# Kernel optimization log

Measured on AMD Instinct MI355X. Metric: run time of the kernel, lower is better.

## Reference

```python
import jax, jax.numpy as jnp
import numpy as np

DIM = 384
NUM_HEADS = 6
HEAD_DIM = DIM // NUM_HEADS
MLP_HIDDEN = 4 * DIM
SCALE = HEAD_DIM ** -0.5
EPS = 1e-5


def layer_norm(x, w, b):
    mu = jnp.mean(x, axis=-1, keepdims=True)
    var = jnp.mean(jnp.square(x - mu), axis=-1, keepdims=True)
    return (x - mu) * jax.lax.rsqrt(var + EPS) * w + b


def setup_inputs() -> dict:
    key = jax.random.key(0)
    ks = jax.random.split(key, 24)
    d = DIM
    s = 0.02
    inp = {
        'x1': jax.random.normal(ks[0], (16, d, 32, 32), jnp.float32),
        'x2': jax.random.normal(ks[1], (16, d, 32, 32), jnp.float32),
        # per-branch attention-input LayerNorm + kqv projection (no bias)
        'ln_a1_w': jnp.ones((d,), jnp.float32), 'ln_a1_b': jnp.zeros((d,), jnp.float32),
        'kqv1_w': jax.random.normal(ks[2], (d, 3 * d), jnp.float32) * s,
        'ln_a2_w': jnp.ones((d,), jnp.float32), 'ln_a2_b': jnp.zeros((d,), jnp.float32),
        'kqv2_w': jax.random.normal(ks[3], (d, 3 * d), jnp.float32) * s,
        # output projections
        'proj1_w': jax.random.normal(ks[4], (d, d), jnp.float32) * s,
        'proj1_b': jnp.zeros((d,), jnp.float32),
        'proj2_w': jax.random.normal(ks[5], (d, d), jnp.float32) * s,
        'proj2_b': jnp.zeros((d,), jnp.float32),
        # post-attention LayerNorms
        'ln1_w': jnp.ones((d,), jnp.float32), 'ln1_b': jnp.zeros((d,), jnp.float32),
        'ln2_w': jnp.ones((d,), jnp.float32), 'ln2_b': jnp.zeros((d,), jnp.float32),
        # MLPs
        'mlp1_fc1_w': jax.random.normal(ks[6], (d, MLP_HIDDEN), jnp.float32) * s,
        'mlp1_fc1_b': jnp.zeros((MLP_HIDDEN,), jnp.float32),
        'mlp1_fc2_w': jax.random.normal(ks[7], (MLP_HIDDEN, d), jnp.float32) * s,
        'mlp1_fc2_b': jnp.zeros((d,), jnp.float32),
        'mlp2_fc1_w': jax.random.normal(ks[8], (d, MLP_HIDDEN), jnp.float32) * s,
        'mlp2_fc1_b': jnp.zeros((MLP_HIDDEN,), jnp.float32),
        'mlp2_fc2_w': jax.random.normal(ks[9], (MLP_HIDDEN, d), jnp.float32) * s,
        'mlp2_fc2_b': jnp.zeros((d,), jnp.float32),
    }
    return inp


def _kqv_branch(x, ln_w, ln_b, Wkqv):
    # x: [B, C, H, W] -> embedding [B, N, C]; k,q,v: [B, h, N, hd]
    B, C, H, W = x.shape
    N = H * W
    emb = x.reshape(B, C, N).transpose(0, 2, 1)
    xn = layer_norm(emb, ln_w, ln_b)
    kqv = (xn @ Wkqv).reshape(B, N, 3, NUM_HEADS, HEAD_DIM).transpose(2, 0, 3, 1, 4)
    return kqv[0], kqv[1], kqv[2], emb


def _cross_attn(q, k, v):
    # q,k,v: [B, h, N, hd] -> [B, N, C]
    scores = jnp.einsum('bhnd,bhmd->bhnm', q, k) * SCALE
    a = jax.nn.softmax(scores, axis=-1)
    o = jnp.einsum('bhnm,bhmd->bhnd', a, v)
    B, h, N, hd = o.shape
    return o.transpose(0, 2, 1, 3).reshape(B, N, h * hd)


def reference(x1, x2, ln_a1_w, ln_a1_b, kqv1_w, ln_a2_w, ln_a2_b, kqv2_w,
              proj1_w, proj1_b, proj2_w, proj2_b, ln1_w, ln1_b, ln2_w, ln2_b,
              mlp1_fc1_w, mlp1_fc1_b, mlp1_fc2_w, mlp1_fc2_b,
              mlp2_fc1_w, mlp2_fc1_b, mlp2_fc2_w, mlp2_fc2_b):
    B, C, H, W = x1.shape
    k1, q1, v1, emb1 = _kqv_branch(x1, ln_a1_w, ln_a1_b, kqv1_w)
    k2, q2, v2, emb2 = _kqv_branch(x2, ln_a2_w, ln_a2_b, kqv2_w)
    a1 = _cross_attn(q1, k2, v2)   # branch 1 queries attend to branch 2
    a2 = _cross_attn(q2, k1, v1)
    out1 = emb1 + (a1 @ proj1_w + proj1_b)
    h1 = layer_norm(out1, ln1_w, ln1_b)
    out1 = out1 + (jax.nn.gelu(h1 @ mlp1_fc1_w + mlp1_fc1_b, approximate=False) @ mlp1_fc2_w + mlp1_fc2_b)
    out2 = emb2 + (a2 @ proj2_w + proj2_b)
    h2 = layer_norm(out2, ln2_w, ln2_b)
    out2 = out2 + (jax.nn.gelu(h2 @ mlp2_fc1_w + mlp2_fc1_b, approximate=False) @ mlp2_fc2_w + mlp2_fc2_b)
    out1 = out1.transpose(0, 2, 1).reshape(B, C, H, W)
    out2 = out2.transpose(0, 2, 1).reshape(B, C, H, W)
    return (out1, out2)
```

## Files before the change

### kernel.cpp

```cpp
#include <hip/hip_runtime.h>
#include <math.h>

typedef unsigned short u16;
typedef __attribute__((ext_vector_type(8))) short short8;
typedef __attribute__((ext_vector_type(4))) float f32x4;

#define MFMA(a,b,c) __builtin_amdgcn_mfma_f32_16x16x32_bf16(a, b, c, 0, 0, 0)
#define SWZ(row, ch) ((((ch) ^ ((row) & 7)) << 3))

__device__ __forceinline__ float b2f(u16 v) {
    union { unsigned int i; float f; } c; c.i = ((unsigned int)v) << 16; return c.f;
}
__device__ __forceinline__ u16 f2b(float f) {
    union { float f; unsigned int i; } c; c.f = f;
    unsigned int u = c.i;
    return (u16)((u + 0x7fffu + ((u >> 16) & 1u)) >> 16);
}

struct TWArgs { const float* src[8]; u16* dst[8]; int K[8]; int N[8]; };

__global__ __launch_bounds__(256) void transpose_w(TWArgs a) {
    int wi = blockIdx.z;
    int K = a.K[wi], N = a.N[wi];
    int n0 = blockIdx.x * 32, k0 = blockIdx.y * 32;
    if (n0 >= N || k0 >= K) return;
    __shared__ float t[32][33];
    const float* s = a.src[wi]; u16* d = a.dst[wi];
    int tx = threadIdx.x & 31, ty = threadIdx.x >> 5;
    for (int i = 0; i < 32; i += 8)
        t[ty + i][tx] = s[(size_t)(k0 + ty + i) * N + n0 + tx];
    __syncthreads();
    for (int i = 0; i < 32; i += 8)
        d[(size_t)(n0 + ty + i) * K + k0 + tx] = f2b(t[tx][ty + i]);
}

__global__ __launch_bounds__(256)
void ln_tr(const float* __restrict__ x0, const float* __restrict__ x1,
           const float* __restrict__ w0, const float* __restrict__ bb0,
           const float* __restrict__ w1, const float* __restrict__ bb1,
           u16* __restrict__ xn0, u16* __restrict__ xn1) {
    int br = blockIdx.z;
    const float* x  = br ? x1 : x0;
    const float* wv = br ? w1 : w0;
    const float* bv = br ? bb1 : bb0;
    u16* xn = br ? xn1 : xn0;
    int b = blockIdx.y, n0 = blockIdx.x * 32;
    __shared__ float tile[32][385];
    __shared__ float smu[32], srs[32];
    int tid = threadIdx.x;
    const float* xb = x + (size_t)b * 384 * 1024 + n0;
    for (int idx = tid; idx < 384 * 32; idx += 256) {
        int c = idx >> 5, nn = idx & 31;
        tile[nn][c] = xb[(size_t)c * 1024 + nn];
    }
    __syncthreads();
    {
        int nn = tid >> 3, part = tid & 7;
        float s1 = 0.f, s2 = 0.f;
        for (int c = part * 48; c < part * 48 + 48; ++c) {
            float v = tile[nn][c]; s1 += v; s2 += v * v;
        }
        for (int off = 1; off < 8; off <<= 1) {
            s1 += __shfl_xor(s1, off, 64); s2 += __shfl_xor(s2, off, 64);
        }
        if (part == 0) {
            float mu = s1 * (1.f / 384.f);
            float var = s2 * (1.f / 384.f) - mu * mu;
            smu[nn] = mu; srs[nn] = rsqrtf(fmaxf(var, 0.f) + 1e-5f);
        }
    }
    __syncthreads();
    size_t rowbase = (size_t)b * 1024 + n0;
    for (int idx = tid; idx < 32 * 384; idx += 256) {
        int nn = idx / 384, c = idx - nn * 384;
        float v = tile[nn][c];
        float g = (v - smu[nn]) * srs[nn] * wv[c] + bv[c];
        xn[(rowbase + nn) * 384 + c] = f2b(g);
    }
}

__global__ __launch_bounds__(256)
void ln_rows(const float* __restrict__ i0, const float* __restrict__ i1,
             const float* __restrict__ w0, const float* __restrict__ bb0,
             const float* __restrict__ w1, const float* __restrict__ bb1,
             u16* __restrict__ o0, u16* __restrict__ o1) {
    int br = blockIdx.z;
    const float* in = br ? i1 : i0;
    const float* wv = br ? w1 : w0;
    const float* bv = br ? bb1 : bb0;
    u16* out = br ? o1 : o0;
    int w = threadIdx.x >> 6, l = threadIdx.x & 63;
    size_t row = (size_t)blockIdx.x * 4 + w;
    const float* p = in + row * 384;
    float v[6]; float s1 = 0.f, s2 = 0.f;
    #pragma unroll
    for (int j = 0; j < 6; j++) { v[j] = p[j * 64 + l]; s1 += v[j]; s2 += v[j] * v[j]; }
    for (int off = 1; off < 64; off <<= 1) {
        s1 += __shfl_xor(s1, off, 64); s2 += __shfl_xor(s2, off, 64);
    }
    float mu = s1 * (1.f / 384.f);
    float var = s2 * (1.f / 384.f) - mu * mu;
    float rs = rsqrtf(fmaxf(var, 0.f) + 1e-5f);
    #pragma unroll
    for (int j = 0; j < 6; j++) {
        int c = j * 64 + l;
        out[row * 384 + c] = f2b((v[j] - mu) * rs * wv[c] + bv[c]);
    }
}

template <int EPI>
__global__ __launch_bounds__(256)
void gemm128(const u16* __restrict__ A0, const u16* __restrict__ A1,
             const u16* __restrict__ B0, const u16* __restrict__ B1,
             void* C0v, void* C1v,
             const float* __restrict__ bias0, const float* __restrict__ bias1,
             const void* R0v, const void* R1v,
             int N, int K) {
    const int br = blockIdx.z;
    const u16* A = br ? A1 : A0;
    const u16* B = br ? B1 : B0;
    void* Cv = br ? C1v : C0v;
    const float* bias = br ? bias1 : bias0;
    const void* Rv = br ? R1v : R0v;

    const int n0 = blockIdx.x * 128;
    const int m0 = blockIdx.y * 128;
    const int tid = threadIdx.x;
    const int w = tid >> 6, l = tid & 63;
    const int wm = w >> 1, wn = w & 1;
    const int lr = l & 15, lq = l >> 4;

    __shared__ alignas(16) u16 As[2][128 * 40];
    __shared__ alignas(16) u16 Bs[2][128 * 40];

    f32x4 acc[4][4];
    #pragma unroll
    for (int i = 0; i < 4; i++)
        #pragma unroll
        for (int j = 0; j < 4; j++) acc[i][j] = (f32x4)0.0f;

    const int ar0 = tid >> 2, ac0 = (tid & 3) * 8;
    const int ar1 = ar0 + 64;
    const u16* Ap0 = A + (size_t)(m0 + ar0) * K + ac0;
    const u16* Ap1 = A + (size_t)(m0 + ar1) * K + ac0;
    const u16* Bp0 = B + (size_t)(n0 + ar0) * K + ac0;
    const u16* Bp1 = B + (size_t)(n0 + ar1) * K + ac0;

    const int nk = K >> 5;
    uint4 pa0 = *(const uint4*)Ap0, pa1 = *(const uint4*)Ap1;
    uint4 pb0 = *(const uint4*)Bp0, pb1 = *(const uint4*)Bp1;
    *(uint4*)&As[0][ar0 * 40 + ac0] = pa0;
    *(uint4*)&As[0][ar1 * 40 + ac0] = pa1;
    *(uint4*)&Bs[0][ar0 * 40 + ac0] = pb0;
    *(uint4*)&Bs[0][ar1 * 40 + ac0] = pb1;
    pa0 = *(const uint4*)(Ap0 + 32); pa1 = *(const uint4*)(Ap1 + 32);
    pb0 = *(const uint4*)(Bp0 + 32); pb1 = *(const uint4*)(Bp1 + 32);
    __syncthreads();

    for (int kt = 0; kt < nk; ++kt) {
        const int cur = kt & 1;
        if (kt + 1 < nk) {
            const int nx = cur ^ 1;
            *(uint4*)&As[nx][ar0 * 40 + ac0] = pa0;
            *(uint4*)&As[nx][ar1 * 40 + ac0] = pa1;
            *(uint4*)&Bs[nx][ar0 * 40 + ac0] = pb0;
            *(uint4*)&Bs[nx][ar1 * 40 + ac0] = pb1;
        }
        if (kt + 2 < nk) {
            const int kb = (kt + 2) * 32;
            pa0 = *(const uint4*)(Ap0 + kb); pa1 = *(const uint4*)(Ap1 + kb);
            pb0 = *(const uint4*)(Bp0 + kb); pb1 = *(const uint4*)(Bp1 + kb);
        }
        short8 af[4], bf[4];
        #pragma unroll
        for (int mt = 0; mt < 4; ++mt)
            af[mt] = *(const short8*)&As[cur][(wm * 64 + mt * 16 + lr) * 40 + lq * 8];
        #pragma unroll
        for (int nt = 0; nt < 4; ++nt)
            bf[nt] = *(const short8*)&Bs[cur][(wn * 64 + nt * 16 + lr) * 40 + lq * 8];
        #pragma unroll
        for (int mt = 0; mt < 4; ++mt)
            #pragma unroll
            for (int nt = 0; nt < 4; ++nt)
                acc[mt][nt] = MFMA(af[mt], bf[nt], acc[mt][nt]);
        __syncthreads();
    }

    #pragma unroll
    for (int mt = 0; mt < 4; ++mt)
        #pragma unroll
        for (int nt = 0; nt < 4; ++nt) {
            const int col = n0 + wn * 64 + nt * 16 + lr;
            const int rbase = m0 + wm * 64 + mt * 16 + lq * 4;
            const float bv = (EPI == 0) ? 0.f : bias[col];
            #pragma unroll
            for (int r = 0; r < 4; r++) {
                const int row = rbase + r;
                const size_t idx = (size_t)row * N + col;
                float v = acc[mt][nt][r];
                if (EPI == 0) {
                    if (col < 768) {
                        ((u16*)Cv)[idx] = f2b(col >= 384 ? v * 0.125f : v);
                    } else {
                        u16* vtb = (u16*)Rv;
                        vtb[((((size_t)(row >> 10)) * 6 + ((col - 768) >> 6)) * 64
                             + (col & 63)) * 1024 + (row & 1023)] = f2b(v);
                    }
                } else if (EPI == 1) {
                    float xr = ((const float*)Rv)[
                        ((size_t)(row >> 10) * 384 + col) * 1024 + (row & 1023)];
                    ((float*)Cv)[idx] = v + bv + xr;
                } else if (EPI == 2) {
                    v += bv;
                    float g = 0.5f * v * (1.f + erff(v * 0.70710678118f));
                    ((u16*)Cv)[idx] = f2b(g);
                } else {
                    ((float*)Cv)[idx] = v + bv + ((const float*)Rv)[idx];
                }
            }
        }
}

__global__ __launch_bounds__(256)
void attn_k(const u16* __restrict__ kqvA, const u16* __restrict__ kqvB,
            const u16* __restrict__ vtA, const u16* __restrict__ vtB,
            u16* __restrict__ oA, u16* __restrict__ oB) {
    const int z = blockIdx.z, b = z >> 1, ob = z & 1;
    const int h = blockIdx.y, qb = blockIdx.x;
    const u16* kqvQ  = (ob ? kqvB : kqvA) + (size_t)b * 1024 * 1152;
    const u16* kqvKV = (ob ? kqvA : kqvB) + (size_t)b * 1024 * 1152;
    const u16* vt    = (ob ? vtA : vtB) + ((size_t)b * 6 + h) * 64 * 1024;
    u16* outp = (ob ? oB : oA) + (size_t)b * 1024 * 384;
    const u16* qp = kqvQ + 384 + h * 64;
    const u16* kp = kqvKV + h * 64;

    __shared__ alignas(16) u16 Qs[128 * 64];
    __shared__ alignas(16) u16 Ks[64 * 64];
    __shared__ alignas(16) u16 Vts[64 * 64];
    __shared__ alignas(16) u16 Ps[4 * 32 * 64];

    const int tid = threadIdx.x, w = tid >> 6, l = tid & 63;
    const int lr = l & 15, lq = l >> 4;
    u16* Psw = Ps + w * 32 * 64;

    #pragma unroll
    for (int i = 0; i < 4; i++) {
        int s = tid + i * 256, row = s >> 3, ch = s & 7;
        *(uint4*)&Qs[row * 64 + SWZ(row, ch)] =
            *(const uint4*)&qp[(size_t)(qb * 128 + row) * 1152 + ch * 8];
    }

    const int srow = tid >> 3, sch = tid & 7;
    uint4 kpre[2], vpre[2];
    #pragma unroll
    for (int i = 0; i < 2; i++) {
        int row = srow + i * 32;
        kpre[i] = *(const uint4*)&kp[(size_t)row * 1152 + sch * 8];
        vpre[i] = *(const uint4*)&vt[(size_t)row * 1024 + sch * 8];
    }

    f32x4 oacc[2][4];
    float psum[2][4];
    #pragma unroll
    for (int a = 0; a < 2; a++)
        #pragma unroll
        for (int n = 0; n < 4; n++) oacc[a][n] = (f32x4)0.0f;
    #pragma unroll
    for (int a = 0; a < 2; a++)
        #pragma unroll
        for (int r = 0; r < 4; r++) psum[a][r] = 0.f;

    for (int jt = 0; jt < 16; ++jt) {
        #pragma unroll
        for (int i = 0; i < 2; i++) {
            int row = srow + i * 32;
            int o = row * 64 + SWZ(row, sch);
            *(uint4*)&Ks[o] = kpre[i];
            *(uint4*)&Vts[o] = vpre[i];
        }
        __syncthreads();
        if (jt < 15) {
            #pragma unroll
            for (int i = 0; i < 2; i++) {
                int row = srow + i * 32;
                kpre[i] = *(const uint4*)&kp[(size_t)((jt + 1) * 64 + row) * 1152 + sch * 8];
                vpre[i] = *(const uint4*)&vt[(size_t)row * 1024 + (jt + 1) * 64 + sch * 8];
            }
        }

        f32x4 sacc[2][4];
        #pragma unroll
        for (int a = 0; a < 2; a++)
            #pragma unroll
            for (int n = 0; n < 4; n++) sacc[a][n] = (f32x4)0.0f;
        #pragma unroll
        for (int ks = 0; ks < 2; ++ks) {
            short8 aq[2], bk[4];
            #pragma unroll
            for (int a = 0; a < 2; a++) {
                int row = w * 32 + a * 16 + lr;
                aq[a] = *(const short8*)&Qs[row * 64 + SWZ(row, ks * 4 + lq)];
            }
            #pragma unroll
            for (int n = 0; n < 4; n++) {
                int row = n * 16 + lr;
                bk[n] = *(const short8*)&Ks[row * 64 + SWZ(row, ks * 4 + lq)];
            }
            #pragma unroll
            for (int a = 0; a < 2; a++)
                #pragma unroll
                for (int n = 0; n < 4; n++) sacc[a][n] = MFMA(aq[a], bk[n], sacc[a][n]);
        }

        #pragma unroll
        for (int a = 0; a < 2; a++)
            #pragma unroll
            for (int r = 0; r < 4; r++) {
                int prow = a * 16 + lq * 4 + r;
                float ps = 0.f;
                #pragma unroll
                for (int n = 0; n < 4; n++) {
                    float p = __expf(sacc[a][n][r]);
                    ps += p;
                    Psw[prow * 64 + ((((2 * n + (lr >> 3)) ^ (prow & 7)) << 3) + (lr & 7))] = f2b(p);
                }
                psum[a][r] += ps;
            }

        #pragma unroll
        for (int ks = 0; ks < 2; ++ks) {
            short8 ap[2], bv4[4];
            #pragma unroll
            for (int a = 0; a < 2; a++) {
                int row = a * 16 + lr;
                ap[a] = *(const short8*)&Psw[row * 64 + SWZ(row, ks * 4 + lq)];
            }
            #pragma unroll
            for (int n = 0; n < 4; n++) {
                int row = n * 16 + lr;
                bv4[n] = *(const short8*)&Vts[row * 64 + SWZ(row, ks * 4 + lq)];
            }
            #pragma unroll
            for (int a = 0; a < 2; a++)
                #pragma unroll
                for (int n = 0; n < 4; n++) oacc[a][n] = MFMA(ap[a], bv4[n], oacc[a][n]);
        }
        __syncthreads();
    }

    #pragma unroll
    for (int a = 0; a < 2; a++)
        #pragma unroll
        for (int r = 0; r < 4; r++) {
            float s = psum[a][r];
            s += __shfl_xor(s, 1, 64); s += __shfl_xor(s, 2, 64);
            s += __shfl_xor(s, 4, 64); s += __shfl_xor(s, 8, 64);
            psum[a][r] = s;
        }
    #pragma unroll
    for (int a = 0; a < 2; a++)
        #pragma unroll
        for (int n = 0; n < 4; n++)
            #pragma unroll
            for (int r = 0; r < 4; r++) {
                size_t row = (size_t)qb * 128 + w * 32 + a * 16 + lq * 4 + r;
                int col = h * 64 + n * 16 + lr;
                outp[row * 384 + col] = f2b(oacc[a][n][r] / psum[a][r]);
            }
}

__global__ __launch_bounds__(256)
void transpose_out(const float* __restrict__ r0, const float* __restrict__ r1,
                   float* __restrict__ out) {
    int z = blockIdx.z, ob = z >> 4, b = z & 15;
    const float* rp = ob ? r1 : r0;
    int c0 = blockIdx.y * 32, n0 = blockIdx.x * 32;
    __shared__ float t[32][33];
    int tx = threadIdx.x & 31, ty = threadIdx.x >> 5;
    for (int i = 0; i < 32; i += 8)
        t[ty + i][tx] = rp[((size_t)b * 1024 + n0 + ty + i) * 384 + c0 + tx];
    __syncthreads();
    for (int i = 0; i < 32; i += 8)
        out[(size_t)ob * 6291456 + ((size_t)b * 384 + c0 + ty + i) * 1024 + n0 + tx]
            = t[tx][ty + i];
}

extern "C" void kernel_launch(void* const* d_in, const int* in_sizes, int n_in,
                              void* d_out, int out_size, void* d_ws, size_t ws_size,
                              hipStream_t stream) {
    const float* x1      = (const float*)d_in[0];
    const float* x2      = (const float*)d_in[1];
    const float* ln_a1_w = (const float*)d_in[2];
    const float* ln_a1_b = (const float*)d_in[3];
    const float* kqv1_w  = (const float*)d_in[4];
    const float* ln_a2_w = (const float*)d_in[5];
    const float* ln_a2_b = (const float*)d_in[6];
    const float* kqv2_w  = (const float*)d_in[7];
    const float* proj1_w = (const float*)d_in[8];
    const float* proj1_b = (const float*)d_in[9];
    const float* proj2_w = (const float*)d_in[10];
    const float* proj2_b = (const float*)d_in[11];
    const float* ln1_w   = (const float*)d_in[12];
    const float* ln1_b   = (const float*)d_in[13];
    const float* ln2_w   = (const float*)d_in[14];
    const float* ln2_b   = (const float*)d_in[15];
    const float* m1f1w   = (const float*)d_in[16];
    const float* m1f1b   = (const float*)d_in[17];
    const float* m1f2w   = (const float*)d_in[18];
    const float* m1f2b   = (const float*)d_in[19];
    const float* m2f1w   = (const float*)d_in[20];
    const float* m2f1b   = (const float*)d_in[21];
    const float* m2f2w   = (const float*)d_in[22];
    const float* m2f2b   = (const float*)d_in[23];
    (void)in_sizes; (void)n_in; (void)out_size; (void)ws_size;

    const size_t R = 16384;
    char* ws = (char*)d_ws;
    size_t off = 0;
    auto alloc = [&](size_t bytes) -> char* {
        char* p = ws + off;
        off = (off + bytes + 255) & ~(size_t)255;
        return p;
    };
    u16* kqv1t  = (u16*)alloc(1152 * 384 * 2);
    u16* kqv2t  = (u16*)alloc(1152 * 384 * 2);
    u16* proj1t = (u16*)alloc(384 * 384 * 2);
    u16* proj2t = (u16*)alloc(384 * 384 * 2);
    u16* fc11t  = (u16*)alloc(1536 * 384 * 2);
    u16* fc12t  = (u16*)alloc(1536 * 384 * 2);
    u16* fc21t  = (u16*)alloc(384 * 1536 * 2);
    u16* fc22t  = (u16*)alloc(384 * 1536 * 2);
    u16* xn1 = (u16*)alloc(R * 384 * 2);
    u16* xn2 = (u16*)alloc(R * 384 * 2);
    char* regC = alloc(R * 1152 * 2 * 2);
    u16* kqv1 = (u16*)regC;
    u16* kqv2 = (u16*)(regC + R * 1152 * 2);
    float* oa1 = (float*)regC;
    float* oa2 = (float*)(regC + R * 384 * 4);
    u16* hid_b2 = (u16*)(regC + 2 * R * 384 * 4);
    u16* at1 = (u16*)d_out;
    u16* at2 = at1 + R * 384;
    u16* vt1 = at2 + R * 384;
    u16* vt2 = vt1 + (size_t)16 * 6 * 64 * 1024;
    u16* hid_b1 = (u16*)d_out;

    TWArgs tw;
    tw.src[0] = kqv1_w;  tw.dst[0] = kqv1t;  tw.K[0] = 384;  tw.N[0] = 1152;
    tw.src[1] = kqv2_w;  tw.dst[1] = kqv2t;  tw.K[1] = 384;  tw.N[1] = 1152;
    tw.src[2] = proj1_w; tw.dst[2] = proj1t; tw.K[2] = 384;  tw.N[2] = 384;
    tw.src[3] = proj2_w; tw.dst[3] = proj2t; tw.K[3] = 384;  tw.N[3] = 384;
    tw.src[4] = m1f1w;   tw.dst[4] = fc11t;  tw.K[4] = 384;  tw.N[4] = 1536;
    tw.src[5] = m2f1w;   tw.dst[5] = fc12t;  tw.K[5] = 384;  tw.N[5] = 1536;
    tw.src[6] = m1f2w;   tw.dst[6] = fc21t;  tw.K[6] = 1536; tw.N[6] = 384;
    tw.src[7] = m2f2w;   tw.dst[7] = fc22t;  tw.K[7] = 1536; tw.N[7] = 384;
    transpose_w<<<dim3(48, 48, 8), dim3(256), 0, stream>>>(tw);

    ln_tr<<<dim3(32, 16, 2), dim3(256), 0, stream>>>(
        x1, x2, ln_a1_w, ln_a1_b, ln_a2_w, ln_a2_b, xn1, xn2);

    gemm128<0><<<dim3(9, 128, 2), dim3(256), 0, stream>>>(
        xn1, xn2, kqv1t, kqv2t, (void*)kqv1, (void*)kqv2,
        (const float*)nullptr, (const float*)nullptr,
        (const void*)vt1, (const void*)vt2, 1152, 384);

    attn_k<<<dim3(8, 6, 32), dim3(256), 0, stream>>>(kqv1, kqv2, vt1, vt2, at1, at2);

    gemm128<1><<<dim3(3, 128, 2), dim3(256), 0, stream>>>(
        at1, at2, proj1t, proj2t, (void*)oa1, (void*)oa2,
        proj1_b, proj2_b, (const void*)x1, (const void*)x2, 384, 384);

    ln_rows<<<dim3(4096, 1, 2), dim3(256), 0, stream>>>(
        oa1, oa2, ln1_w, ln1_b, ln2_w, ln2_b, xn1, xn2);

    for (int half = 0; half < 2; ++half) {
        const size_t ro = (size_t)half * 8192;
        gemm128<2><<<dim3(12, 64, 2), dim3(256), 0, stream>>>(
            xn1 + ro * 384, xn2 + ro * 384, fc11t, fc12t,
            (void*)hid_b1, (void*)hid_b2, m1f1b, m2f1b, nullptr, nullptr, 1536, 384);
        gemm128<3><<<dim3(3, 64, 2), dim3(256), 0, stream>>>(
            hid_b1, hid_b2, fc21t, fc22t,
            (void*)(oa1 + ro * 384), (void*)(oa2 + ro * 384),
            m1f2b, m2f2b, (const void*)(oa1 + ro * 384), (const void*)(oa2 + ro * 384),
            384, 1536);
    }

    transpose_out<<<dim3(32, 12, 32), dim3(256), 0, stream>>>(oa1, oa2, (float*)d_out);
}
```

Before: 649.7 us.

## Deepen K/V prefetch, remap attention grid for XCD locality, use exp2 softmax

```diff
diff --git a/kernel.cpp b/kernel.cpp
--- a/kernel.cpp
+++ b/kernel.cpp
@@ -7,6 +7,7 @@
 
 #define MFMA(a,b,c) __builtin_amdgcn_mfma_f32_16x16x32_bf16(a, b, c, 0, 0, 0)
 #define SWZ(row, ch) ((((ch) ^ ((row) & 7)) << 3))
+#define EXP2F(x) __builtin_amdgcn_exp2f(x)
 
 __device__ __forceinline__ float b2f(u16 v) {
     union { unsigned int i; float f; } c; c.i = ((unsigned int)v) << 16; return c.f;
@@ -15,6 +16,10 @@
     union { float f; unsigned int i; } c; c.f = f;
     unsigned int u = c.i;
     return (u16)((u + 0x7fffu + ((u >> 16) & 1u)) >> 16);
+}
+__device__ __forceinline__ u16 f2b_p(float f) {
+    union { float f; unsigned int i; } c; c.f = f;
+    return (u16)((c.i + 0x8000u) >> 16);
 }
 
 struct TWArgs { const float* src[8]; u16* dst[8]; int K[8]; int N[8]; };
@@ -200,7 +205,7 @@
                 float v = acc[mt][nt][r];
                 if (EPI == 0) {
                     if (col < 768) {
-                        ((u16*)Cv)[idx] = f2b(col >= 384 ? v * 0.125f : v);
+                        ((u16*)Cv)[idx] = f2b(col >= 384 ? v * 0.18033688f : v);
                     } else {
                         u16* vtb = (u16*)Rv;
                         vtb[((((size_t)(row >> 10)) * 6 + ((col - 768) >> 6)) * 64
@@ -225,8 +230,11 @@
 void attn_k(const u16* __restrict__ kqvA, const u16* __restrict__ kqvB,
             const u16* __restrict__ vtA, const u16* __restrict__ vtB,
             u16* __restrict__ oA, u16* __restrict__ oB) {
-    const int z = blockIdx.z, b = z >> 1, ob = z & 1;
-    const int h = blockIdx.y, qb = blockIdx.x;
+    const int bid = blockIdx.x;
+    const int g = bid & 7, qb = (bid >> 3) & 7, s = bid >> 6;
+    const int grp = s * 8 + g;
+    const int ob = grp & 1, h = (grp >> 1) % 6, b = grp / 12;
+
     const u16* kqvQ  = (ob ? kqvB : kqvA) + (size_t)b * 1024 * 1152;
     const u16* kqvKV = (ob ? kqvA : kqvB) + (size_t)b * 1024 * 1152;
     const u16* vt    = (ob ? vtA : vtB) + ((size_t)b * 6 + h) * 64 * 1024;
@@ -245,19 +253,21 @@
 
     #pragma unroll
     for (int i = 0; i < 4; i++) {
-        int s = tid + i * 256, row = s >> 3, ch = s & 7;
+        int si = tid + i * 256, row = si >> 3, ch = si & 7;
         *(uint4*)&Qs[row * 64 + SWZ(row, ch)] =
             *(const uint4*)&qp[(size_t)(qb * 128 + row) * 1152 + ch * 8];
     }
 
     const int srow = tid >> 3, sch = tid & 7;
-    uint4 kpre[2], vpre[2];
-    #pragma unroll
-    for (int i = 0; i < 2; i++) {
-        int row = srow + i * 32;
-        kpre[i] = *(const uint4*)&kp[(size_t)row * 1152 + sch * 8];
-        vpre[i] = *(const uint4*)&vt[(size_t)row * 1024 + sch * 8];
-    }
+    uint4 kpre[2][2], vpre[2][2];
+    #pragma unroll
+    for (int t = 0; t < 2; t++)
+        #pragma unroll
+        for (int i = 0; i < 2; i++) {
+            int row = srow + i * 32;
+            kpre[t][i] = *(const uint4*)&kp[(size_t)(t * 64 + row) * 1152 + sch * 8];
+            vpre[t][i] = *(const uint4*)&vt[(size_t)row * 1024 + t * 64 + sch * 8];
+        }
 
     f32x4 oacc[2][4];
     float psum[2][4];
@@ -271,20 +281,21 @@
         for (int r = 0; r < 4; r++) psum[a][r] = 0.f;
 
     for (int jt = 0; jt < 16; ++jt) {
+        const int slot = jt & 1;
         #pragma unroll
         for (int i = 0; i < 2; i++) {
             int row = srow + i * 32;
             int o = row * 64 + SWZ(row, sch);
-            *(uint4*)&Ks[o] = kpre[i];
-            *(uint4*)&Vts[o] = vpre[i];
+            *(uint4*)&Ks[o] = kpre[slot][i];
+            *(uint4*)&Vts[o] = vpre[slot][i];
         }
         __syncthreads();
-        if (jt < 15) {
+        if (jt + 2 < 16) {
             #pragma unroll
             for (int i = 0; i < 2; i++) {
                 int row = srow + i * 32;
-                kpre[i] = *(const uint4*)&kp[(size_t)((jt + 1) * 64 + row) * 1152 + sch * 8];
-                vpre[i] = *(const uint4*)&vt[(size_t)row * 1024 + (jt + 1) * 64 + sch * 8];
+                kpre[slot][i] = *(const uint4*)&kp[(size_t)((jt + 2) * 64 + row) * 1152 + sch * 8];
+                vpre[slot][i] = *(const uint4*)&vt[(size_t)row * 1024 + (jt + 2) * 64 + sch * 8];
             }
         }
 
@@ -320,9 +331,9 @@
                 float ps = 0.f;
                 #pragma unroll
                 for (int n = 0; n < 4; n++) {
-                    float p = __expf(sacc[a][n][r]);
+                    float p = EXP2F(sacc[a][n][r]);
                     ps += p;
-                    Psw[prow * 64 + ((((2 * n + (lr >> 3)) ^ (prow & 7)) << 3) + (lr & 7))] = f2b(p);
+                    Psw[prow * 64 + ((((2 * n + (lr >> 3)) ^ (prow & 7)) << 3) + (lr & 7))] = f2b_p(p);
                 }
                 psum[a][r] += ps;
             }
@@ -352,10 +363,10 @@
     for (int a = 0; a < 2; a++)
         #pragma unroll
         for (int r = 0; r < 4; r++) {
-            float s = psum[a][r];
-            s += __shfl_xor(s, 1, 64); s += __shfl_xor(s, 2, 64);
-            s += __shfl_xor(s, 4, 64); s += __shfl_xor(s, 8, 64);
-            psum[a][r] = s;
+            float sm = psum[a][r];
+            sm += __shfl_xor(sm, 1, 64); sm += __shfl_xor(sm, 2, 64);
+            sm += __shfl_xor(sm, 4, 64); sm += __shfl_xor(sm, 8, 64);
+            psum[a][r] = sm;
         }
     #pragma unroll
     for (int a = 0; a < 2; a++)
@@ -463,7 +474,7 @@
         (const float*)nullptr, (const float*)nullptr,
         (const void*)vt1, (const void*)vt2, 1152, 384);
 
-    attn_k<<<dim3(8, 6, 32), dim3(256), 0, stream>>>(kqv1, kqv2, vt1, vt2, at1, at2);
+    attn_k<<<dim3(1536), dim3(256), 0, stream>>>(kqv1, kqv2, vt1, vt2, at1, at2);
 
     gemm128<1><<<dim3(3, 128, 2), dim3(256), 0, stream>>>(
         at1, at2, proj1t, proj2t, (void*)oa1, (void*)oa2,
```

Result: faster. 626.8 us (-3.5%).
